# Kernel tuning notes

Measured on AMD Instinct MI355X. Metric: run time of the kernel, lower is better.

The kernel has to match this reference:

```python
import jax, jax.numpy as jnp
import numpy as np

BANDWIDTH = 1.0


def setup_inputs() -> dict:
    key = jax.random.key(0)
    k1, k2, k3 = jax.random.split(key, 3)
    test_Xs = jax.random.normal(k1, (2048, 64), dtype=jnp.float32)
    train_Xs = jax.random.normal(k2, (4096, 64), dtype=jnp.float32)
    weights = jax.random.uniform(k3, (4096,), dtype=jnp.float32)
    return {"test_Xs": test_Xs, "train_Xs": train_Xs, "weights": weights}


def reference(test_Xs, train_Xs, weights):
    # Gaussian KDE: log p(x_i) = logsumexp_j( -0.5 * ||w_j (x_i - y_j) / h||^2 - Z )
    # Since w_j is a scalar per train point, ||w_j (x_i - y_j)||^2 = w_j^2 * ||x_i - y_j||^2,
    # so we compute pairwise squared distances via the GEMM expansion instead of
    # materializing the [n_test, n_train, d] diff tensor.
    n, d = train_Xs.shape
    h = jnp.float32(BANDWIDTH)
    Z = 0.5 * d * jnp.log(2.0 * jnp.float32(np.pi)) + d * jnp.log(h) + jnp.log(jnp.float32(n))

    test_sq = jnp.sum(test_Xs * test_Xs, axis=-1, keepdims=True)        # [nt, 1]
    train_sq = jnp.sum(train_Xs * train_Xs, axis=-1)[None, :]           # [1, ntr]
    cross = jnp.einsum("td,nd->tn", test_Xs, train_Xs)                  # [nt, ntr]
    dist2 = test_sq - 2.0 * cross + train_sq                            # [nt, ntr]
    dist2 = jnp.maximum(dist2, 0.0)

    scale = (weights / h) ** 2                                           # [ntr]
    log_exp = -0.5 * dist2 * scale[None, :]                              # [nt, ntr]
    return jax.nn.logsumexp(log_exp - Z, axis=-1)                        # [nt]
```

## Files before the change

### kernel.cpp

```cpp
#include <hip/hip_runtime.h>
#include <hip/hip_bf16.h>
#include <math.h>

typedef __attribute__((ext_vector_type(8))) short short8;
typedef __attribute__((ext_vector_type(4))) float f32x4;

#define LOG2E 1.44269504088896340736f

__global__ __launch_bounds__(256) void kde_prep(
    const float* __restrict__ testX, const float* __restrict__ trainX,
    const float* __restrict__ w,
    __hip_bfloat16* __restrict__ testbf, __hip_bfloat16* __restrict__ trainbf,
    float* __restrict__ sqx, float* __restrict__ sqy, float* __restrict__ nhs,
    float* __restrict__ out_sum, int n_test, int n_train)
{
    int gw = blockIdx.x * 4 + (threadIdx.x >> 6);
    int lane = threadIdx.x & 63;
    if (gw < n_test) {
        int i = gw;
        float x = testX[i * 64 + lane];
        testbf[i * 64 + lane] = __float2bfloat16(x);
        float s = x * x;
        #pragma unroll
        for (int m = 1; m < 64; m <<= 1) s += __shfl_xor(s, m);
        if (lane == 0) { sqx[i] = s; out_sum[i] = 0.0f; }
    } else if (gw < n_test + n_train) {
        int j = gw - n_test;
        float y = trainX[j * 64 + lane];
        trainbf[j * 64 + lane] = __float2bfloat16(y);
        float s = y * y;
        #pragma unroll
        for (int m = 1; m < 64; m <<= 1) s += __shfl_xor(s, m);
        if (lane == 0) {
            sqy[j] = s;
            float ww = w[j];
            nhs[j] = -0.5f * LOG2E * ww * ww;
        }
    }
}

__global__ __launch_bounds__(256) void kde_main(
    const __hip_bfloat16* __restrict__ testbf,
    const __hip_bfloat16* __restrict__ trainbf,
    const float* __restrict__ sqx, const float* __restrict__ sqy,
    const float* __restrict__ nhs, float* __restrict__ out_sum)
{
    const int mbase = blockIdx.x * 16;
    const int wv    = threadIdx.x >> 6;
    const int lane  = threadIdx.x & 63;
    const int cg    = lane & 15;
    const int kg    = lane >> 4;

    const int arow = mbase + cg;
    short8 a0 = *(const short8*)(testbf + arow * 64 +      kg * 8);
    short8 a1 = *(const short8*)(testbf + arow * 64 + 32 + kg * 8);

    float sxr[4];
    #pragma unroll
    for (int r = 0; r < 4; ++r) sxr[r] = sqx[mbase + kg * 4 + r];

    float s[4] = {0.f, 0.f, 0.f, 0.f};
    const int colchunk = blockIdx.y * 512 + wv * 128;

    #pragma unroll
    for (int step = 0; step < 8; ++step) {
        const int bcol = colchunk + step * 16 + cg;
        short8 b0 = *(const short8*)(trainbf + bcol * 64 +      kg * 8);
        short8 b1 = *(const short8*)(trainbf + bcol * 64 + 32 + kg * 8);

        f32x4 acc = {0.f, 0.f, 0.f, 0.f};
        acc = __builtin_amdgcn_mfma_f32_16x16x32_bf16(a0, b0, acc, 0, 0, 0);
        acc = __builtin_amdgcn_mfma_f32_16x16x32_bf16(a1, b1, acc, 0, 0, 0);

        const float sy = sqy[bcol];
        const float nh = nhs[bcol];
        #pragma unroll
        for (int r = 0; r < 4; ++r) {
            float d2 = fmaxf(sxr[r] + sy - 2.0f * acc[r], 0.0f);
            s[r] += exp2f(d2 * nh);
        }
    }

    #pragma unroll
    for (int m = 1; m < 16; m <<= 1) {
        #pragma unroll
        for (int r = 0; r < 4; ++r) s[r] += __shfl_xor(s[r], m);
    }
    if (cg == 0) {
        #pragma unroll
        for (int r = 0; r < 4; ++r)
            atomicAdd(&out_sum[mbase + kg * 4 + r], s[r]);
    }
}

__global__ __launch_bounds__(256) void kde_final(
    const float* __restrict__ out_sum, float* __restrict__ out, float Z, int n)
{
    int i = blockIdx.x * 256 + threadIdx.x;
    if (i < n) out[i] = logf(out_sum[i]) - Z;
}

extern "C" void kernel_launch(void* const* d_in, const int* in_sizes, int n_in,
                              void* d_out, int out_size, void* d_ws, size_t ws_size,
                              hipStream_t stream) {
    const float* testX  = (const float*)d_in[0];
    const float* trainX = (const float*)d_in[1];
    const float* w      = (const float*)d_in[2];
    float* out = (float*)d_out;

    const int d = 64;
    const int n_test  = in_sizes[0] / d;
    const int n_train = in_sizes[1] / d;

    char* ws = (char*)d_ws;
    size_t off = 0;
    __hip_bfloat16* testbf  = (__hip_bfloat16*)(ws + off); off += (size_t)n_test  * d * 2;
    __hip_bfloat16* trainbf = (__hip_bfloat16*)(ws + off); off += (size_t)n_train * d * 2;
    float* sqx     = (float*)(ws + off); off += (size_t)n_test  * 4;
    float* sqy     = (float*)(ws + off); off += (size_t)n_train * 4;
    float* nhs     = (float*)(ws + off); off += (size_t)n_train * 4;
    float* out_sum = (float*)(ws + off); off += (size_t)n_test  * 4;
    (void)ws_size; (void)n_in; (void)out_size;

    const float Z = 0.5f * d * logf(2.0f * (float)M_PI) + logf((float)n_train);

    const int rows = n_test + n_train;
    kde_prep<<<(rows + 3) / 4, 256, 0, stream>>>(
        testX, trainX, w, testbf, trainbf, sqx, sqy, nhs, out_sum, n_test, n_train);

    dim3 grid(n_test / 16, n_train / 512);
    kde_main<<<grid, 256, 0, stream>>>(testbf, trainbf, sqx, sqy, nhs, out_sum);

    kde_final<<<(n_test + 255) / 256, 256, 0, stream>>>(out_sum, out, Z, n_test);
}
```

Baseline: 24.58 us.

## Fuse final log into main kernel via last-block counter; vectorize prep

Removes the separate finalize launch. Each row group now keeps an atomic counter, and the last column block to finish computes log(sum) - Z for its 16 rows. The prep kernel is rewritten so each wave handles four rows using float4 loads and 4-wide bf16 stores, and it also zeroes the counters. This cuts one kernel launch and the prep instruction count, in exchange for a threadfence plus a counter atomic in every main block.

```diff
diff --git a/kernel.cpp b/kernel.cpp
--- a/kernel.cpp
+++ b/kernel.cpp
@@ -3,38 +3,57 @@
 #include <math.h>
 
 typedef __attribute__((ext_vector_type(8))) short short8;
+typedef __attribute__((ext_vector_type(4))) short short4v;
 typedef __attribute__((ext_vector_type(4))) float f32x4;
 
 #define LOG2E 1.44269504088896340736f
+
+__device__ __forceinline__ short bf16bits(float x) {
+    __hip_bfloat16 b = __float2bfloat16(x);
+    short r;
+    __builtin_memcpy(&r, &b, 2);
+    return r;
+}
 
 __global__ __launch_bounds__(256) void kde_prep(
     const float* __restrict__ testX, const float* __restrict__ trainX,
     const float* __restrict__ w,
     __hip_bfloat16* __restrict__ testbf, __hip_bfloat16* __restrict__ trainbf,
     float* __restrict__ sqx, float* __restrict__ sqy, float* __restrict__ nhs,
-    float* __restrict__ out_sum, int n_test, int n_train)
+    float* __restrict__ out_sum, int* __restrict__ counters,
+    int n_test, int n_train, int n_groups)
 {
-    int gw = blockIdx.x * 4 + (threadIdx.x >> 6);
-    int lane = threadIdx.x & 63;
-    if (gw < n_test) {
-        int i = gw;
-        float x = testX[i * 64 + lane];
-        testbf[i * 64 + lane] = __float2bfloat16(x);
-        float s = x * x;
-        #pragma unroll
-        for (int m = 1; m < 64; m <<= 1) s += __shfl_xor(s, m);
-        if (lane == 0) { sqx[i] = s; out_sum[i] = 0.0f; }
-    } else if (gw < n_test + n_train) {
-        int j = gw - n_test;
-        float y = trainX[j * 64 + lane];
-        trainbf[j * 64 + lane] = __float2bfloat16(y);
-        float s = y * y;
-        #pragma unroll
-        for (int m = 1; m < 64; m <<= 1) s += __shfl_xor(s, m);
-        if (lane == 0) {
-            sqy[j] = s;
-            float ww = w[j];
-            nhs[j] = -0.5f * LOG2E * ww * ww;
+    const int tid  = threadIdx.x;
+    const int zi = blockIdx.x * 256 + tid;
+    if (zi < n_test) out_sum[zi] = 0.0f;
+    else if (zi < n_test + n_groups) counters[zi - n_test] = 0;
+
+    const int wid  = blockIdx.x * 4 + (tid >> 6);
+    const int lane = tid & 63;
+    const int sub  = lane >> 4;
+    const int q    = lane & 15;
+    const int row  = wid * 4 + sub;
+
+    const float* src;
+    __hip_bfloat16* dst;
+    int r_local;
+    if (row < n_test) { src = testX; dst = testbf; r_local = row; }
+    else              { src = trainX; dst = trainbf; r_local = row - n_test; }
+    if (row >= n_test + n_train) return;
+
+    const float4 v = ((const float4*)src)[r_local * 16 + q];
+    short4v b = { bf16bits(v.x), bf16bits(v.y), bf16bits(v.z), bf16bits(v.w) };
+    *(short4v*)(dst + r_local * 64 + q * 4) = b;
+
+    float s = v.x * v.x + v.y * v.y + v.z * v.z + v.w * v.w;
+    #pragma unroll
+    for (int m = 1; m < 16; m <<= 1) s += __shfl_xor(s, m);
+    if (q == 0) {
+        if (row < n_test) sqx[r_local] = s;
+        else {
+            sqy[r_local] = s;
+            float ww = w[r_local];
+            nhs[r_local] = -0.5f * LOG2E * ww * ww;
         }
     }
 }
@@ -43,7 +62,8 @@
     const __hip_bfloat16* __restrict__ testbf,
     const __hip_bfloat16* __restrict__ trainbf,
     const float* __restrict__ sqx, const float* __restrict__ sqy,
-    const float* __restrict__ nhs, float* __restrict__ out_sum)
+    const float* __restrict__ nhs, float* __restrict__ out_sum,
+    int* __restrict__ counters, float* __restrict__ out, float Z)
 {
     const int mbase = blockIdx.x * 16;
     const int wv    = threadIdx.x >> 6;
@@ -91,13 +111,20 @@
         for (int r = 0; r < 4; ++r)
             atomicAdd(&out_sum[mbase + kg * 4 + r], s[r]);
     }
-}
 
-__global__ __launch_bounds__(256) void kde_final(
-    const float* __restrict__ out_sum, float* __restrict__ out, float Z, int n)
-{
-    int i = blockIdx.x * 256 + threadIdx.x;
-    if (i < n) out[i] = logf(out_sum[i]) - Z;
+    __shared__ int sflag;
+    __threadfence();
+    __syncthreads();
+    if (threadIdx.x == 0) {
+        int old = atomicAdd(&counters[blockIdx.x], 1);
+        sflag = (old == (int)gridDim.y - 1) ? 1 : 0;
+    }
+    __syncthreads();
+    if (sflag && threadIdx.x < 16) {
+        float ssum = __hip_atomic_load(&out_sum[mbase + threadIdx.x],
+                                       __ATOMIC_RELAXED, __HIP_MEMORY_SCOPE_AGENT);
+        out[mbase + threadIdx.x] = logf(ssum) - Z;
+    }
 }
 
 extern "C" void kernel_launch(void* const* d_in, const int* in_sizes, int n_in,
@@ -111,6 +138,7 @@
     const int d = 64;
     const int n_test  = in_sizes[0] / d;
     const int n_train = in_sizes[1] / d;
+    const int n_groups = n_test / 16;
 
     char* ws = (char*)d_ws;
     size_t off = 0;
@@ -120,16 +148,17 @@
     float* sqy     = (float*)(ws + off); off += (size_t)n_train * 4;
     float* nhs     = (float*)(ws + off); off += (size_t)n_train * 4;
     float* out_sum = (float*)(ws + off); off += (size_t)n_test  * 4;
+    int*   counters = (int*)(ws + off);  off += (size_t)n_groups * 4;
     (void)ws_size; (void)n_in; (void)out_size;
 
     const float Z = 0.5f * d * logf(2.0f * (float)M_PI) + logf((float)n_train);
 
     const int rows = n_test + n_train;
-    kde_prep<<<(rows + 3) / 4, 256, 0, stream>>>(
-        testX, trainX, w, testbf, trainbf, sqx, sqy, nhs, out_sum, n_test, n_train);
+    kde_prep<<<rows / 16, 256, 0, stream>>>(
+        testX, trainX, w, testbf, trainbf, sqx, sqy, nhs,
+        out_sum, counters, n_test, n_train, n_groups);
 
-    dim3 grid(n_test / 16, n_train / 512);
-    kde_main<<<grid, 256, 0, stream>>>(testbf, trainbf, sqx, sqy, nhs, out_sum);
-
-    kde_final<<<(n_test + 255) / 256, 256, 0, stream>>>(out_sum, out, Z, n_test);
+    dim3 grid(n_groups, n_train / 512);
+    kde_main<<<grid, 256, 0, stream>>>(
+        testbf, trainbf, sqx, sqy, nhs, out_sum, counters, out, Z);
 }
```

Result: slower. 80.21 us (+226.3%).
